# Performance work log

Measured on AMD Instinct MI355X. Metric: run time of the kernel, lower is better.

The kernel has to match this reference:

```python
import jax, jax.numpy as jnp
import numpy as np

# dims: batch, token counts, feature dims, hidden d, glimpses
B, VN, QN, AN = 16, 96, 96, 96
VD = QD = AD = 256
HD, G = 128, 2
W_STD = 0.02


def setup_inputs() -> dict:
    key = jax.random.key(0)
    ks = jax.random.split(key, 24)
    f32 = jnp.float32
    def w(k, shape):
        return jax.random.normal(k, shape, f32) * W_STD
    return {
        'v': jax.random.normal(ks[0], (B, VN, VD), f32),
        'q': jax.random.normal(ks[1], (B, QN, QD), f32),
        'a': jax.random.normal(ks[2], (B, AN, AD), f32),
        # TCNet tucker projections (FCNet: Linear + ReLU)
        'Wvt': w(ks[3], (VD, HD)), 'bvt': jnp.zeros((HD,), f32),
        'Wqt': w(ks[4], (QD, HD)), 'bqt': jnp.zeros((HD,), f32),
        'Wat': w(ks[5], (AD, HD)), 'bat': jnp.zeros((HD,), f32),
        # trilinear core mapping shared hidden dim -> glimpses
        'Wg': w(ks[6], (HD, G)),
        # value projections (plain Linear, *_dim -> h_dim)
        'Wvp': w(ks[7], (VD, HD)), 'bvp': jnp.zeros((HD,), f32),
        'Wqp': w(ks[8], (QD, HD)), 'bqp': jnp.zeros((HD,), f32),
        'Wap': w(ks[9], (AD, HD)), 'bap': jnp.zeros((HD,), f32),
        # residual updates (glimpse*h_dim -> *_dim)
        'Wvu': w(ks[10], (G * HD, VD)), 'bvu': jnp.zeros((VD,), f32),
        'Wqu': w(ks[11], (G * HD, QD)), 'bqu': jnp.zeros((QD,), f32),
        'Wau': w(ks[12], (G * HD, AD)), 'bau': jnp.zeros((AD,), f32),
    }


def reference(v, q, a,
              Wvt, bvt, Wqt, bqt, Wat, bat, Wg,
              Wvp, bvp, Wqp, bqp, Wap, bap,
              Wvu, bvu, Wqu, bqu, Wau, bau):
    b = v.shape[0]
    # --- TCNet (reconstructed trilinear scorer): tucker proj + rank-1 core ---
    vt = jax.nn.relu(v @ Wvt + bvt)               # [b, vn, h]
    qt = jax.nn.relu(q @ Wqt + bqt)               # [b, qn, h]
    at = jax.nn.relu(a @ Wat + bat)               # [b, an, h]
    logits = jnp.einsum('bvh,bqh,bah,hg->bvqag', vt, qt, at, Wg)
    z = vt.sum(1) * qt.sum(1) * at.sum(1)         # pooled trilinear embedding [b, h]
    # --- mask padded v tokens (rows whose abs-sum is 0), softmax over v*q*a ---
    mask = (jnp.abs(v).sum(2) == 0)[:, :, None, None, None]
    logits = jnp.where(mask, -jnp.inf, logits)
    p = jax.nn.softmax(logits.reshape(b, -1, G), axis=1).reshape(logits.shape)
    # --- value projections + broadcast-sum combinations ---
    vp = v @ Wvp + bvp                            # [b, vn, d]
    qp = q @ Wqp + bqp                            # [b, qn, d]
    ap = a @ Wap + bap                            # [b, an, d]
    qa = qp[:, :, None, :] + ap[:, None, :, :]    # [b, qn, an, d]
    va = vp[:, :, None, :] + ap[:, None, :, :]    # [b, vn, an, d]
    vq = vp[:, :, None, :] + qp[:, None, :, :]    # [b, vn, qn, d]
    # --- three attended contractions + residual linear updates (eval: no dropout) ---
    c_v = jnp.einsum('bvqag,bqad->bvdg', p, qa)
    c_v = jnp.swapaxes(c_v, 2, 3).reshape(b, v.shape[1], G * HD)  # permute(0,1,3,2).view
    updated_v = v + c_v @ Wvu + bvu
    c_q = jnp.einsum('bvqag,bvad->bqdg', p, va)
    c_q = jnp.swapaxes(c_q, 2, 3).reshape(b, q.shape[1], G * HD)
    updated_q = q + c_q @ Wqu + bqu
    c_a = jnp.einsum('bvqag,bvqd->bagd', p, vq)   # note: torch einsum emits [b,a,g,d]
    c_a = jnp.swapaxes(c_a, 2, 3).reshape(b, a.shape[1], HD * G)  # then permute(0,1,3,2).view
    updated_a = a + c_a @ Wau + bau
    return jnp.stack([updated_v, updated_q, updated_a])  # [3, b, n, dim]
```

## Files before the change

kernel.cpp:

```cpp
#include <hip/hip_runtime.h>


#define B_  16
#define N_  96
#define D_  256
#define H_  128
#define CV  4
#define NCH 24
#define PAD 136

typedef _Float16 f16x8 __attribute__((ext_vector_type(8)));
typedef float f32x4_t  __attribute__((ext_vector_type(4)));

__device__ __forceinline__ float bf2f(unsigned short u) {
    union { unsigned u32; float f; } x;
    x.u32 = ((unsigned)u) << 16;
    return x.f;
}

__global__ __launch_bounds__(256) void k_proj(
    const float* __restrict__ v, const float* __restrict__ q,
    const float* __restrict__ a,
    const float* __restrict__ Wvt, const float* __restrict__ bvt,
    const float* __restrict__ Wqt, const float* __restrict__ bqt,
    const float* __restrict__ Wat, const float* __restrict__ bat,
    const float* __restrict__ Wvp, const float* __restrict__ bvp,
    const float* __restrict__ Wqp, const float* __restrict__ bqp,
    const float* __restrict__ Wap, const float* __restrict__ bap,
    const float* __restrict__ Wg,
    _Float16* __restrict__ vtg_o, _Float16* __restrict__ qt_o,
    _Float16* __restrict__ at_o,
    float* __restrict__ vp_o, float* __restrict__ qp_o, float* __restrict__ ap_o)
{
    int wg = blockIdx.x;
    int tc = wg % 8, b = (wg / 8) & 15, p = wg / 128;
    const float* xs_[6] = {v, q, a, v, q, a};
    const float* Ws_[6] = {Wvt, Wqt, Wat, Wvp, Wqp, Wap};
    const float* bs_[6] = {bvt, bqt, bat, bvp, bqp, bap};

    __shared__ __align__(16) float x_l[12 * D_];

    int tid = threadIdx.x;
    int t0 = tc * 12;
    const float* x = xs_[p] + (size_t)(b * N_ + t0) * D_;
    for (int i = tid; i < 768; i += 256)
        ((float4*)x_l)[i] = ((const float4*)x)[i];
    __syncthreads();

    int d = tid & 127, tg = tid >> 7;
    const float* W = Ws_[p];
    float bias = bs_[p][d];
    float acc[6];
#pragma unroll
    for (int t = 0; t < 6; t++) acc[t] = bias;

    for (int kb = 0; kb < 32; kb++) {
        int k = kb * 8;
        float w0 = W[(k + 0) * H_ + d], w1 = W[(k + 1) * H_ + d];
        float w2 = W[(k + 2) * H_ + d], w3 = W[(k + 3) * H_ + d];
        float w4 = W[(k + 4) * H_ + d], w5 = W[(k + 5) * H_ + d];
        float w6 = W[(k + 6) * H_ + d], w7 = W[(k + 7) * H_ + d];
#pragma unroll
        for (int t = 0; t < 6; t++) {
            int lt = tg * 6 + t;
            float4 xa = *(const float4*)&x_l[lt * D_ + k];
            float4 xb = *(const float4*)&x_l[lt * D_ + k + 4];
            acc[t] += xa.x * w0 + xa.y * w1 + xa.z * w2 + xa.w * w3
                    + xb.x * w4 + xb.y * w5 + xb.z * w6 + xb.w * w7;
        }
    }

    int trow = b * N_ + t0 + tg * 6;
    if (p == 0) {
        float wg0 = Wg[d * 2 + 0], wg1 = Wg[d * 2 + 1];
#pragma unroll
        for (int t = 0; t < 6; t++) {
            float r = fmaxf(acc[t], 0.f);
            _Float16* vg = vtg_o + (size_t)(trow + t) * 2 * H_;
            vg[d]      = (_Float16)(r * wg0);
            vg[H_ + d] = (_Float16)(r * wg1);
        }
    } else if (p < 3) {
        _Float16* o = (p == 1) ? qt_o : at_o;
#pragma unroll
        for (int t = 0; t < 6; t++)
            o[(trow + t) * H_ + d] = (_Float16)fmaxf(acc[t], 0.f);
    } else {
        float* outs[3] = {vp_o, qp_o, ap_o};
        float* o = outs[p - 3];
#pragma unroll
        for (int t = 0; t < 6; t++) o[(trow + t) * H_ + d] = acc[t];
    }
}

__global__ __launch_bounds__(256) void k_logits(
    const _Float16* __restrict__ vtg, const _Float16* __restrict__ qt,
    const _Float16* __restrict__ at,
    float* __restrict__ Evq_part, float* __restrict__ Eva_part,
    unsigned short* __restrict__ E_qa_part)
{
    int bid = blockIdx.x;
    int g = bid & 1, vc = (bid >> 1) % NCH, b = bid / (2 * NCH);
    int tid = threadIdx.x;

    __shared__ __align__(16) _Float16 qt_l[N_ * PAD];
    __shared__ __align__(16) _Float16 at_l[N_ * PAD];

    const _Float16* qtb = qt + (size_t)b * N_ * H_;
    const _Float16* atb = at + (size_t)b * N_ * H_;

    for (int it = 0; it < 12; it++) {
        int i = tid + it * 256;
        int e = i * 4, t = e >> 7, h = e & 127;
        *(ushort4*)&qt_l[t * PAD + h] = *(const ushort4*)&qtb[e];
        *(ushort4*)&at_l[t * PAD + h] = *(const ushort4*)&atb[e];
    }
    __syncthreads();

    int wave = tid >> 6, lane = tid & 63, quad = lane >> 4, l15 = lane & 15;
    int qi0 = (wave >> 1) * 3, aj0 = (wave & 1) * 3;

    float eqa[3][3][4];
#pragma unroll
    for (int i = 0; i < 3; i++)
#pragma unroll
        for (int j = 0; j < 3; j++)
#pragma unroll
            for (int r = 0; r < 4; r++) eqa[i][j][r] = 0.f;

    for (int vl = 0; vl < CV; vl++) {
        int vrow = vc * CV + vl;
        const _Float16* vgp = vtg + ((size_t)(b * N_ + vrow) * 2 + g) * H_;

        f32x4_t acc[3][3];
#pragma unroll
        for (int i = 0; i < 3; i++)
#pragma unroll
            for (int j = 0; j < 3; j++)
                acc[i][j] = (f32x4_t){0.f, 0.f, 0.f, 0.f};

#pragma unroll
        for (int ks = 0; ks < 4; ks++) {
            f16x8 v8 = *(const f16x8*)&vgp[ks * 32 + quad * 8];
            f16x8 af[3], bfr[3];
#pragma unroll
            for (int i = 0; i < 3; i++)
                af[i] = *(const f16x8*)&qt_l[((qi0 + i) * 16 + l15) * PAD + ks * 32 + quad * 8];
#pragma unroll
            for (int jt = 0; jt < 3; jt++) {
                f16x8 raw = *(const f16x8*)&at_l[((aj0 + jt) * 16 + l15) * PAD + ks * 32 + quad * 8];
                bfr[jt] = raw * v8;
            }
#pragma unroll
            for (int i = 0; i < 3; i++)
#pragma unroll
                for (int jt = 0; jt < 3; jt++)
                    acc[i][jt] = __builtin_amdgcn_mfma_f32_16x16x32_f16(af[i], bfr[jt], acc[i][jt], 0, 0, 0);
        }

        float s[3][4];
        float c[3];
#pragma unroll
        for (int i = 0; i < 3; i++) {
            s[i][0] = 0.f; s[i][1] = 0.f; s[i][2] = 0.f; s[i][3] = 0.f;
        }
        c[0] = 0.f; c[1] = 0.f; c[2] = 0.f;
#pragma unroll
        for (int i = 0; i < 3; i++)
#pragma unroll
            for (int jt = 0; jt < 3; jt++) {
                float e0 = __expf(fminf(fmaxf(acc[i][jt][0], -30.f), 30.f));
                float e1 = __expf(fminf(fmaxf(acc[i][jt][1], -30.f), 30.f));
                float e2 = __expf(fminf(fmaxf(acc[i][jt][2], -30.f), 30.f));
                float e3 = __expf(fminf(fmaxf(acc[i][jt][3], -30.f), 30.f));
                eqa[i][jt][0] += e0; eqa[i][jt][1] += e1;
                eqa[i][jt][2] += e2; eqa[i][jt][3] += e3;
                s[i][0] += e0; s[i][1] += e1; s[i][2] += e2; s[i][3] += e3;
                c[jt] += e0 + e1 + e2 + e3;
            }

        float* evqp = Evq_part + ((size_t)bid * CV + vl) * 192 + (wave & 1) * 96;
#pragma unroll
        for (int i = 0; i < 3; i++) {
            float s0 = s[i][0], s1 = s[i][1], s2 = s[i][2], s3 = s[i][3];
#pragma unroll
            for (int m = 1; m < 16; m <<= 1) {
                s0 += __shfl_xor(s0, m); s1 += __shfl_xor(s1, m);
                s2 += __shfl_xor(s2, m); s3 += __shfl_xor(s3, m);
            }
            if (l15 == 0) {
                int qr = (qi0 + i) * 16 + quad * 4;
                evqp[qr + 0] = s0; evqp[qr + 1] = s1;
                evqp[qr + 2] = s2; evqp[qr + 3] = s3;
            }
        }
        float* evap = Eva_part + ((size_t)bid * CV + vl) * 192 + (wave >> 1) * 96;
#pragma unroll
        for (int jt = 0; jt < 3; jt++) {
            float cs = c[jt];
            cs += __shfl_xor(cs, 16);
            cs += __shfl_xor(cs, 32);
            if (lane < 16) evap[(aj0 + jt) * 16 + l15] = cs;
        }
    }

    unsigned short* Pp = E_qa_part + (size_t)bid * 9216;
#pragma unroll
    for (int i = 0; i < 3; i++)
#pragma unroll
        for (int jt = 0; jt < 3; jt++)
#pragma unroll
            for (int r = 0; r < 4; r++) {
                int idx = (i * 3 + jt) * 4 + r;
                union { float f; unsigned u; } x;
                x.f = eqa[i][jt][r];
                unsigned rr = x.u + 0x7fffu + ((x.u >> 16) & 1u);
                Pp[idx * 256 + tid] = (unsigned short)(rr >> 16);
            }
}

__global__ __launch_bounds__(256) void k_mid(
    const unsigned short* __restrict__ E_qa_part,
    const float* __restrict__ Evq_part, const float* __restrict__ Eva_part,
    float* __restrict__ E_qa, float* __restrict__ E_vq,
    float* __restrict__ E_va, float* __restrict__ Zinv)
{
    int wg = blockIdx.x;
    int tid = threadIdx.x;
    if (wg < 1152) {
        int idx = wg % 36, bg = wg / 36;
        int b = bg >> 1, g = bg & 1;
        float s = 0.f;
        const unsigned short* Pp = E_qa_part + ((size_t)(b * 2 * NCH + g)) * 9216 + idx * 256 + tid;
#pragma unroll
        for (int vc = 0; vc < NCH; vc++) s += bf2f(Pp[(size_t)vc * 2 * 9216]);

        int wave = tid >> 6, lane = tid & 63, quad = lane >> 4, l15 = lane & 15;
        int qi0 = (wave >> 1) * 3, aj0 = (wave & 1) * 3;
        int i = idx / 12, jt = (idx / 4) % 3, r = idx & 3;
        int qq = (qi0 + i) * 16 + quad * 4 + r;
        int aa = (aj0 + jt) * 16 + l15;
        E_qa[(size_t)bg * 9216 + qq * 96 + aa] = s;
    } else {
        int bg = wg - 1152;
        int b = bg >> 1, g = bg & 1;
        float z = 0.f;
        for (int i = tid; i < 9216; i += 256) {
            int vrow = i / 96, col = i - vrow * 96;
            int vc = vrow / CV, vl = vrow - vc * CV;
            size_t pb = ((size_t)(b * 2 * NCH + vc * 2 + g) * CV + vl) * 192;
            float s1 = Evq_part[pb + col] + Evq_part[pb + 96 + col];
            E_vq[(b * 2 + g) * 9216 + i] = s1;
            z += s1;
            float s2 = Eva_part[pb + col] + Eva_part[pb + 96 + col];
            E_va[(b * 2 + g) * 9216 + i] = s2;
        }
        __shared__ float red[256];
        red[tid] = z;
        __syncthreads();
        for (int s = 128; s > 0; s >>= 1) {
            if (tid < s) red[tid] += red[tid + s];
            __syncthreads();
        }
        if (tid == 0) Zinv[b * 2 + g] = 1.f / fmaxf(red[0], 1e-30f);
    }
}

__global__ __launch_bounds__(256) void k_ctxup(
    const float* __restrict__ E_vq, const float* __restrict__ E_va,
    const float* __restrict__ E_qa,
    const float* __restrict__ vp, const float* __restrict__ qp,
    const float* __restrict__ ap, const float* __restrict__ Zinv,
    const float* __restrict__ v, const float* __restrict__ q,
    const float* __restrict__ a,
    const float* __restrict__ Wvu, const float* __restrict__ bvu,
    const float* __restrict__ Wqu, const float* __restrict__ bqu,
    const float* __restrict__ Wau, const float* __restrict__ bau,
    float* __restrict__ out)
{
    int wg = blockIdx.x;
    int tc = wg % 24, b = (wg / 24) & 15, o = wg / 384;
    int tid = threadIdx.x;
    int t0 = tc * 4;

    __shared__ __align__(16) float E1l[2][4 * 100];
    __shared__ __align__(16) float E2l[2][4 * 100];
    __shared__ __align__(16) float c_l[4 * 256];

    for (int i = tid; i < 768; i += 256) {
        int g2 = i / 384, rem = i - g2 * 384;
        int t = rem / 96, j = rem - t * 96;
        const float* Evq = E_vq + (b * 2 + g2) * 9216;
        const float* Eva = E_va + (b * 2 + g2) * 9216;
        const float* Eqa = E_qa + (b * 2 + g2) * 9216;
        float e1, e2;
        if (o == 0)      { e1 = Evq[(t0 + t) * 96 + j]; e2 = Eva[(t0 + t) * 96 + j]; }
        else if (o == 1) { e1 = Evq[j * 96 + t0 + t];   e2 = Eqa[(t0 + t) * 96 + j]; }
        else             { e1 = Eva[j * 96 + t0 + t];   e2 = Eqa[j * 96 + t0 + t]; }
        E1l[g2][t * 100 + j] = e1;
        E2l[g2][t * 100 + j] = e2;
    }
    __syncthreads();

    {
        int d = tid & 127, g2 = tid >> 7;
        const float* P1 = ((o == 0) ? qp : vp) + b * N_ * H_;
        const float* P2 = ((o == 2) ? qp : ap) + b * N_ * H_;
        float acc[4] = {0.f, 0.f, 0.f, 0.f};
        for (int jb = 0; jb < 24; jb++) {
            int j4 = jb * 4;
            float p10 = P1[(j4 + 0) * H_ + d], p11 = P1[(j4 + 1) * H_ + d];
            float p12 = P1[(j4 + 2) * H_ + d], p13 = P1[(j4 + 3) * H_ + d];
            float p20 = P2[(j4 + 0) * H_ + d], p21 = P2[(j4 + 1) * H_ + d];
            float p22 = P2[(j4 + 2) * H_ + d], p23 = P2[(j4 + 3) * H_ + d];
#pragma unroll
            for (int t8 = 0; t8 < 4; t8++) {
                float4 e1 = *(const float4*)&E1l[g2][t8 * 100 + j4];
                float4 e2 = *(const float4*)&E2l[g2][t8 * 100 + j4];
                acc[t8] += e1.x * p10 + e1.y * p11 + e1.z * p12 + e1.w * p13
                         + e2.x * p20 + e2.y * p21 + e2.z * p22 + e2.w * p23;
            }
        }
        float zi = Zinv[b * 2 + g2];
        int col = (o == 2) ? (d * 2 + g2) : (g2 * 128 + d);
#pragma unroll
        for (int t8 = 0; t8 < 4; t8++)
            c_l[t8 * 256 + col] = acc[t8] * zi;
    }
    __syncthreads();

    const float* xs_[3] = {v, q, a};
    const float* Ws_[3] = {Wvu, Wqu, Wau};
    const float* bs_[3] = {bvu, bqu, bau};
    const float* W = Ws_[o];
    const float* x = xs_[o] + (size_t)(b * N_ + t0) * 256;
    float bias = bs_[o][tid];
    float acc[4];
#pragma unroll
    for (int t = 0; t < 4; t++) acc[t] = bias + x[t * 256 + tid];

    for (int kb = 0; kb < 64; kb++) {
        int k = kb * 4;
        float w0 = W[(k + 0) * 256 + tid];
        float w1 = W[(k + 1) * 256 + tid];
        float w2 = W[(k + 2) * 256 + tid];
        float w3 = W[(k + 3) * 256 + tid];
#pragma unroll
        for (int t = 0; t < 4; t++) {
            float4 c4 = *(const float4*)&c_l[t * 256 + k];
            acc[t] += c4.x * w0 + c4.y * w1 + c4.z * w2 + c4.w * w3;
        }
    }
    float* ob = out + (size_t)((o * B_ + b) * N_ + t0) * 256;
#pragma unroll
    for (int t = 0; t < 4; t++) ob[t * 256 + tid] = acc[t];
}

extern "C" void kernel_launch(void* const* d_in, const int* in_sizes, int n_in,
                              void* d_out, int out_size, void* d_ws, size_t ws_size,
                              hipStream_t stream)
{
    const float* v   = (const float*)d_in[0];
    const float* q   = (const float*)d_in[1];
    const float* a   = (const float*)d_in[2];
    const float* Wvt = (const float*)d_in[3];
    const float* bvt = (const float*)d_in[4];
    const float* Wqt = (const float*)d_in[5];
    const float* bqt = (const float*)d_in[6];
    const float* Wat = (const float*)d_in[7];
    const float* bat = (const float*)d_in[8];
    const float* Wg  = (const float*)d_in[9];
    const float* Wvp = (const float*)d_in[10];
    const float* bvp = (const float*)d_in[11];
    const float* Wqp = (const float*)d_in[12];
    const float* bqp = (const float*)d_in[13];
    const float* Wap = (const float*)d_in[14];
    const float* bap = (const float*)d_in[15];
    const float* Wvu = (const float*)d_in[16];
    const float* bvu = (const float*)d_in[17];
    const float* Wqu = (const float*)d_in[18];
    const float* bqu = (const float*)d_in[19];
    const float* Wau = (const float*)d_in[20];
    const float* bau = (const float*)d_in[21];

    char* ws = (char*)d_ws;
    size_t off = 0;
    auto alloc = [&](size_t bytes) {
        char* p = ws + off;
        off += (bytes + 255) & ~(size_t)255;
        return (void*)p;
    };
    _Float16* vtg = (_Float16*)alloc((size_t)B_ * N_ * 2 * H_ * 2);
    _Float16* qt  = (_Float16*)alloc((size_t)B_ * N_ * H_ * 2);
    _Float16* at  = (_Float16*)alloc((size_t)B_ * N_ * H_ * 2);
    float* vpb  = (float*)alloc((size_t)B_ * N_ * H_ * 4);
    float* qpb  = (float*)alloc((size_t)B_ * N_ * H_ * 4);
    float* apb  = (float*)alloc((size_t)B_ * N_ * H_ * 4);
    float* E_vq = (float*)alloc((size_t)B_ * 2 * 9216 * 4);
    float* E_va = (float*)alloc((size_t)B_ * 2 * 9216 * 4);
    float* E_qa = (float*)alloc((size_t)B_ * 2 * 9216 * 4);
    float* Zinv = (float*)alloc(256);
    float* Evq_part = (float*)alloc((size_t)768 * CV * 192 * 4);
    float* Eva_part = (float*)alloc((size_t)768 * CV * 192 * 4);
    unsigned short* E_qa_part =
        (unsigned short*)alloc((size_t)B_ * NCH * 2 * 9216 * 2);

    k_proj<<<768, 256, 0, stream>>>(v, q, a, Wvt, bvt, Wqt, bqt, Wat, bat,
                                    Wvp, bvp, Wqp, bqp, Wap, bap, Wg,
                                    vtg, qt, at, vpb, qpb, apb);
    k_logits<<<B_ * NCH * 2, 256, 0, stream>>>(vtg, qt, at,
                                               Evq_part, Eva_part, E_qa_part);
    k_mid<<<1184, 256, 0, stream>>>(E_qa_part, Evq_part, Eva_part,
                                    E_qa, E_vq, E_va, Zinv);
    k_ctxup<<<1152, 256, 0, stream>>>(E_vq, E_va, E_qa, vpb, qpb, apb, Zinv,
                                      v, q, a, Wvu, bvu, Wqu, bqu, Wau, bau,
                                      (float*)d_out);
}
```

Baseline: 198.5 us.

## Use fp16 transposed projections and weights with fdot2 in context-update kernel

k_proj now writes the value projections in fp16, transposed to [b,h,n], and k_mid gains extra blocks that transpose the update weights into fp16 [out,k]. k_ctxup then reads contiguous f16x8 vectors, and both of its contractions use packed fp16 dot2 instructions in place of scalar fp32 FMAs. The aim is to cut memory traffic and instruction count in the context and update phases. The cost is lower precision for the E tiles, the context vectors and the weights. The weights are also re-transposed on every call, and each thread's strided 16-byte loads may coalesce poorly.

```diff
diff --git a/kernel.cpp b/kernel.cpp
--- a/kernel.cpp
+++ b/kernel.cpp
@@ -10,6 +10,7 @@
 #define PAD 136
 
 typedef _Float16 f16x8 __attribute__((ext_vector_type(8)));
+typedef _Float16 f16x2 __attribute__((ext_vector_type(2)));
 typedef float f32x4_t  __attribute__((ext_vector_type(4)));
 
 __device__ __forceinline__ float bf2f(unsigned short u) {
@@ -30,7 +31,8 @@
     const float* __restrict__ Wg,
     _Float16* __restrict__ vtg_o, _Float16* __restrict__ qt_o,
     _Float16* __restrict__ at_o,
-    float* __restrict__ vp_o, float* __restrict__ qp_o, float* __restrict__ ap_o)
+    _Float16* __restrict__ vpT, _Float16* __restrict__ qpT,
+    _Float16* __restrict__ apT)
 {
     int wg = blockIdx.x;
     int tc = wg % 8, b = (wg / 8) & 15, p = wg / 128;
@@ -86,10 +88,10 @@
         for (int t = 0; t < 6; t++)
             o[(trow + t) * H_ + d] = (_Float16)fmaxf(acc[t], 0.f);
     } else {
-        float* outs[3] = {vp_o, qp_o, ap_o};
-        float* o = outs[p - 3];
-#pragma unroll
-        for (int t = 0; t < 6; t++) o[(trow + t) * H_ + d] = acc[t];
+        _Float16* outs[3] = {vpT, qpT, apT};
+        _Float16* oP = outs[p - 3] + ((size_t)(b * H_ + d)) * N_ + t0 + tg * 6;
+#pragma unroll
+        for (int t = 0; t < 6; t++) oP[t] = (_Float16)acc[t];
     }
 }
 
@@ -222,8 +224,11 @@
 __global__ __launch_bounds__(256) void k_mid(
     const unsigned short* __restrict__ E_qa_part,
     const float* __restrict__ Evq_part, const float* __restrict__ Eva_part,
+    const float* __restrict__ Wvu, const float* __restrict__ Wqu,
+    const float* __restrict__ Wau,
     float* __restrict__ E_qa, float* __restrict__ E_vq,
-    float* __restrict__ E_va, float* __restrict__ Zinv)
+    float* __restrict__ E_va, float* __restrict__ Zinv,
+    _Float16* __restrict__ WT)
 {
     int wg = blockIdx.x;
     int tid = threadIdx.x;
@@ -241,7 +246,7 @@
         int qq = (qi0 + i) * 16 + quad * 4 + r;
         int aa = (aj0 + jt) * 16 + l15;
         E_qa[(size_t)bg * 9216 + qq * 96 + aa] = s;
-    } else {
+    } else if (wg < 1184) {
         int bg = wg - 1152;
         int b = bg >> 1, g = bg & 1;
         float z = 0.f;
@@ -263,19 +268,30 @@
             __syncthreads();
         }
         if (tid == 0) Zinv[b * 2 + g] = 1.f / fmaxf(red[0], 1e-30f);
+    } else {
+        int t = wg - 1184;
+        int w = t / 32, ks = t % 32;
+        const float* Ws[3] = {Wvu, Wqu, Wau};
+        const float* W = Ws[w];
+        _Float16* WTw = WT + (size_t)w * 65536;
+#pragma unroll
+        for (int kk = 0; kk < 8; kk++) {
+            int k = ks * 8 + kk;
+            WTw[(size_t)tid * 256 + k] = (_Float16)W[k * 256 + tid];
+        }
     }
 }
 
 __global__ __launch_bounds__(256) void k_ctxup(
     const float* __restrict__ E_vq, const float* __restrict__ E_va,
     const float* __restrict__ E_qa,
-    const float* __restrict__ vp, const float* __restrict__ qp,
-    const float* __restrict__ ap, const float* __restrict__ Zinv,
+    const _Float16* __restrict__ vpT, const _Float16* __restrict__ qpT,
+    const _Float16* __restrict__ apT, const float* __restrict__ Zinv,
     const float* __restrict__ v, const float* __restrict__ q,
     const float* __restrict__ a,
-    const float* __restrict__ Wvu, const float* __restrict__ bvu,
-    const float* __restrict__ Wqu, const float* __restrict__ bqu,
-    const float* __restrict__ Wau, const float* __restrict__ bau,
+    const _Float16* __restrict__ WT,
+    const float* __restrict__ bvu, const float* __restrict__ bqu,
+    const float* __restrict__ bau,
     float* __restrict__ out)
 {
     int wg = blockIdx.x;
@@ -283,9 +299,9 @@
     int tid = threadIdx.x;
     int t0 = tc * 4;
 
-    __shared__ __align__(16) float E1l[2][4 * 100];
-    __shared__ __align__(16) float E2l[2][4 * 100];
-    __shared__ __align__(16) float c_l[4 * 256];
+    __shared__ __align__(16) _Float16 E1l[2][4][96];
+    __shared__ __align__(16) _Float16 E2l[2][4][96];
+    __shared__ __align__(16) _Float16 c_l[4][256];
 
     for (int i = tid; i < 768; i += 256) {
         int g2 = i / 384, rem = i - g2 * 384;
@@ -297,58 +313,55 @@
         if (o == 0)      { e1 = Evq[(t0 + t) * 96 + j]; e2 = Eva[(t0 + t) * 96 + j]; }
         else if (o == 1) { e1 = Evq[j * 96 + t0 + t];   e2 = Eqa[(t0 + t) * 96 + j]; }
         else             { e1 = Eva[j * 96 + t0 + t];   e2 = Eqa[j * 96 + t0 + t]; }
-        E1l[g2][t * 100 + j] = e1;
-        E2l[g2][t * 100 + j] = e2;
+        E1l[g2][t][j] = (_Float16)e1;
+        E2l[g2][t][j] = (_Float16)e2;
     }
     __syncthreads();
 
     {
         int d = tid & 127, g2 = tid >> 7;
-        const float* P1 = ((o == 0) ? qp : vp) + b * N_ * H_;
-        const float* P2 = ((o == 2) ? qp : ap) + b * N_ * H_;
-        float acc[4] = {0.f, 0.f, 0.f, 0.f};
-        for (int jb = 0; jb < 24; jb++) {
-            int j4 = jb * 4;
-            float p10 = P1[(j4 + 0) * H_ + d], p11 = P1[(j4 + 1) * H_ + d];
-            float p12 = P1[(j4 + 2) * H_ + d], p13 = P1[(j4 + 3) * H_ + d];
-            float p20 = P2[(j4 + 0) * H_ + d], p21 = P2[(j4 + 1) * H_ + d];
-            float p22 = P2[(j4 + 2) * H_ + d], p23 = P2[(j4 + 3) * H_ + d];
-#pragma unroll
-            for (int t8 = 0; t8 < 4; t8++) {
-                float4 e1 = *(const float4*)&E1l[g2][t8 * 100 + j4];
-                float4 e2 = *(const float4*)&E2l[g2][t8 * 100 + j4];
-                acc[t8] += e1.x * p10 + e1.y * p11 + e1.z * p12 + e1.w * p13
-                         + e2.x * p20 + e2.y * p21 + e2.z * p22 + e2.w * p23;
+        const _Float16* P1 = ((o == 0) ? qpT : vpT) + ((size_t)(b * H_ + d)) * N_;
+        const _Float16* P2 = ((o == 2) ? qpT : apT) + ((size_t)(b * H_ + d)) * N_;
+        float acc4[4] = {0.f, 0.f, 0.f, 0.f};
+        for (int jb = 0; jb < 12; jb++) {
+            f16x8 p1 = *(const f16x8*)&P1[jb * 8];
+            f16x8 p2 = *(const f16x8*)&P2[jb * 8];
+#pragma unroll
+            for (int t = 0; t < 4; t++) {
+                f16x8 e1 = *(const f16x8*)&E1l[g2][t][jb * 8];
+                f16x8 e2 = *(const f16x8*)&E2l[g2][t][jb * 8];
+#pragma unroll
+                for (int pp = 0; pp < 4; pp++) {
+                    acc4[t] = __builtin_amdgcn_fdot2(((f16x2*)&e1)[pp], ((f16x2*)&p1)[pp], acc4[t], false);
+                    acc4[t] = __builtin_amdgcn_fdot2(((f16x2*)&e2)[pp], ((f16x2*)&p2)[pp], acc4[t], false);
+                }
             }
         }
         float zi = Zinv[b * 2 + g2];
         int col = (o == 2) ? (d * 2 + g2) : (g2 * 128 + d);
 #pragma unroll
-        for (int t8 = 0; t8 < 4; t8++)
-            c_l[t8 * 256 + col] = acc[t8] * zi;
+        for (int t = 0; t < 4; t++)
+            c_l[t][col] = (_Float16)(acc4[t] * zi);
     }
     __syncthreads();
 
     const float* xs_[3] = {v, q, a};
-    const float* Ws_[3] = {Wvu, Wqu, Wau};
     const float* bs_[3] = {bvu, bqu, bau};
-    const float* W = Ws_[o];
     const float* x = xs_[o] + (size_t)(b * N_ + t0) * 256;
+    const _Float16* Wn = WT + (size_t)o * 65536 + (size_t)tid * 256;
     float bias = bs_[o][tid];
     float acc[4];
 #pragma unroll
     for (int t = 0; t < 4; t++) acc[t] = bias + x[t * 256 + tid];
 
-    for (int kb = 0; kb < 64; kb++) {
-        int k = kb * 4;
-        float w0 = W[(k + 0) * 256 + tid];
-        float w1 = W[(k + 1) * 256 + tid];
-        float w2 = W[(k + 2) * 256 + tid];
-        float w3 = W[(k + 3) * 256 + tid];
+    for (int kb = 0; kb < 32; kb++) {
+        f16x8 w8 = *(const f16x8*)&Wn[kb * 8];
 #pragma unroll
         for (int t = 0; t < 4; t++) {
-            float4 c4 = *(const float4*)&c_l[t * 256 + k];
-            acc[t] += c4.x * w0 + c4.y * w1 + c4.z * w2 + c4.w * w3;
+            f16x8 c8 = *(const f16x8*)&c_l[t][kb * 8];
+#pragma unroll
+            for (int pp = 0; pp < 4; pp++)
+                acc[t] = __builtin_amdgcn_fdot2(((f16x2*)&c8)[pp], ((f16x2*)&w8)[pp], acc[t], false);
         }
     }
     float* ob = out + (size_t)((o * B_ + b) * N_ + t0) * 256;
@@ -393,9 +406,9 @@
     _Float16* vtg = (_Float16*)alloc((size_t)B_ * N_ * 2 * H_ * 2);
     _Float16* qt  = (_Float16*)alloc((size_t)B_ * N_ * H_ * 2);
     _Float16* at  = (_Float16*)alloc((size_t)B_ * N_ * H_ * 2);
-    float* vpb  = (float*)alloc((size_t)B_ * N_ * H_ * 4);
-    float* qpb  = (float*)alloc((size_t)B_ * N_ * H_ * 4);
-    float* apb  = (float*)alloc((size_t)B_ * N_ * H_ * 4);
+    _Float16* vpT = (_Float16*)alloc((size_t)B_ * H_ * N_ * 2);
+    _Float16* qpT = (_Float16*)alloc((size_t)B_ * H_ * N_ * 2);
+    _Float16* apT = (_Float16*)alloc((size_t)B_ * H_ * N_ * 2);
     float* E_vq = (float*)alloc((size_t)B_ * 2 * 9216 * 4);
     float* E_va = (float*)alloc((size_t)B_ * 2 * 9216 * 4);
     float* E_qa = (float*)alloc((size_t)B_ * 2 * 9216 * 4);
@@ -404,15 +417,17 @@
     float* Eva_part = (float*)alloc((size_t)768 * CV * 192 * 4);
     unsigned short* E_qa_part =
         (unsigned short*)alloc((size_t)B_ * NCH * 2 * 9216 * 2);
+    _Float16* WT = (_Float16*)alloc((size_t)3 * 256 * 256 * 2);
 
     k_proj<<<768, 256, 0, stream>>>(v, q, a, Wvt, bvt, Wqt, bqt, Wat, bat,
                                     Wvp, bvp, Wqp, bqp, Wap, bap, Wg,
-                                    vtg, qt, at, vpb, qpb, apb);
+                                    vtg, qt, at, vpT, qpT, apT);
     k_logits<<<B_ * NCH * 2, 256, 0, stream>>>(vtg, qt, at,
                                                Evq_part, Eva_part, E_qa_part);
-    k_mid<<<1184, 256, 0, stream>>>(E_qa_part, Evq_part, Eva_part,
-                                    E_qa, E_vq, E_va, Zinv);
-    k_ctxup<<<1152, 256, 0, stream>>>(E_vq, E_va, E_qa, vpb, qpb, apb, Zinv,
-                                      v, q, a, Wvu, bvu, Wqu, bqu, Wau, bau,
+    k_mid<<<1280, 256, 0, stream>>>(E_qa_part, Evq_part, Eva_part,
+                                    Wvu, Wqu, Wau,
+                                    E_qa, E_vq, E_va, Zinv, WT);
+    k_ctxup<<<1152, 256, 0, stream>>>(E_vq, E_va, E_qa, vpT, qpT, apT, Zinv,
+                                      v, q, a, WT, bvu, bqu, bau,
                                       (float*)d_out);
 }
```

Result: slower. 210.0 us (+5.8%).
